# Optimization experiments

Measured on AMD Instinct MI355X. Metric: run time of the kernel, lower is better.

The kernel has to match this reference:

```python
import jax, jax.numpy as jnp
import numpy as np

N_NODES = 100000
N_EDGES = 1600000
IN_CH, HID, EMB = 128, 64, 32


def _glorot(key, shape):
    lim = np.sqrt(6.0 / (shape[0] + shape[1])).astype(np.float32)
    return jax.random.uniform(key, shape, jnp.float32, -lim, lim)


def setup_inputs() -> dict:
    key = jax.random.key(0)
    ks = jax.random.split(key, 5)
    x = jax.random.normal(ks[0], (N_NODES, IN_CH), dtype=jnp.float32)
    edges = jax.random.randint(ks[1], (2, N_EDGES), 0, N_NODES)
    W1 = _glorot(ks[2], (IN_CH, HID)); b1 = jnp.zeros((HID,), jnp.float32)
    W2 = _glorot(ks[3], (HID, EMB)); b2 = jnp.zeros((EMB,), jnp.float32)
    W3 = _glorot(ks[4], (HID, EMB)); b3 = jnp.zeros((EMB,), jnp.float32)
    return {"x": x, "edges": edges, "W1": W1, "b1": b1,
            "W2": W2, "b2": b2, "W3": W3, "b3": b3}


def reference(x, edges, W1, b1, W2, b2, W3, b3):
    N = x.shape[0]
    # GCNConv default: add self-loops, symmetric D^-1/2 A D^-1/2 normalization
    loop = jnp.arange(N, dtype=edges.dtype)
    src = jnp.concatenate([edges[0], loop])  # [E+N] message sources
    dst = jnp.concatenate([edges[1], loop])  # [E+N] message targets
    deg = jax.ops.segment_sum(jnp.ones_like(dst, dtype=x.dtype), dst, num_segments=N)
    dinv = jnp.where(deg > 0, jax.lax.rsqrt(deg), 0.0)
    norm = dinv[src] * dinv[dst]  # [E+N], cached across the three convs (cached=True)

    def gcn(h, W, b):
        h = h @ W                                  # [N, out]
        msg = h[src] * norm[:, None]               # gather + edge scale
        return jax.ops.segment_sum(msg, dst, num_segments=N) + b  # scatter-add

    h = jax.nn.relu(gcn(x, W1, b1))
    return gcn(h, W2, b2), gcn(h, W3, b3)
```

## Files before the change

### kernel.cpp

```cpp
#include <hip/hip_runtime.h>

#define NN 100000
#define NE 1600000
#define NB 391
#define CHUNK 4096
#define NCHUNK 391

typedef __attribute__((ext_vector_type(8))) short short8_t;
typedef __attribute__((ext_vector_type(4))) float float4_t;

__device__ inline unsigned short f2bf(float f) {
    unsigned int u = __float_as_uint(f);
    unsigned int r = u + 0x7fffu + ((u >> 16) & 1u);
    return (unsigned short)(r >> 16);
}
__device__ inline float bf_lo(unsigned int u) { return __uint_as_float(u << 16); }
__device__ inline float bf_hi(unsigned int u) { return __uint_as_float(u & 0xffff0000u); }

__global__ __launch_bounds__(256) void k_hist(const int* __restrict__ dst,
                                              int* __restrict__ bhist) {
    __shared__ int lh[NB];
    int t = threadIdx.x;
    for (int i = t; i < NB; i += 256) lh[i] = 0;
    __syncthreads();
    for (int e = blockIdx.x * 256 + t; e < NE; e += 256 * 256)
        atomicAdd(&lh[dst[e] >> 8], 1);
    __syncthreads();
    for (int i = t; i < NB; i += 256)
        if (lh[i]) atomicAdd(&bhist[i], lh[i]);
}

__global__ __launch_bounds__(256) void k_scanb(const int* __restrict__ bhist,
                                               int* __restrict__ boff,
                                               int* __restrict__ bcur) {
    __shared__ int sh[256];
    int t = threadIdx.x;
    int base = t * 2;
    int v0 = (base + 0 < NB) ? bhist[base + 0] : 0;
    int v1 = (base + 1 < NB) ? bhist[base + 1] : 0;
    int tsum = v0 + v1;
    sh[t] = tsum;
    __syncthreads();
    for (int d = 1; d < 256; d <<= 1) {
        int x = (t >= d) ? sh[t - d] : 0;
        __syncthreads();
        sh[t] += x;
        __syncthreads();
    }
    int excl = sh[t] - tsum;
    if (base + 0 < NB) { boff[base + 0] = excl;      bcur[base + 0] = excl; }
    if (base + 1 < NB) { boff[base + 1] = excl + v0; bcur[base + 1] = excl + v0; }
    if (t == 255) boff[NB] = sh[255];
}

__global__ __launch_bounds__(512) void k_bscatter(const int* __restrict__ src,
                                                  const int* __restrict__ dst,
                                                  int* __restrict__ bcur,
                                                  unsigned int* __restrict__ pairs) {
    __shared__ int lh[NB];
    __shared__ int lbase[NB];
    int t = threadIdx.x;
    int e0 = blockIdx.x * CHUNK;
    int e1 = min(e0 + CHUNK, NE);
    for (int i = t; i < NB; i += 512) lh[i] = 0;
    __syncthreads();
    for (int e = e0 + t; e < e1; e += 512)
        atomicAdd(&lh[dst[e] >> 8], 1);
    __syncthreads();
    int rot = (int)((blockIdx.x * 97u) % NB);
    for (int i = t; i < NB; i += 512) {
        int ii = i + rot; if (ii >= NB) ii -= NB;
        int h = lh[ii];
        lbase[ii] = h ? atomicAdd(&bcur[ii], h) : 0;
    }
    __syncthreads();
    for (int i = t; i < NB; i += 512) lh[i] = 0;
    __syncthreads();
    for (int e = e0 + t; e < e1; e += 512) {
        int d = dst[e];
        int b = d >> 8;
        int r = atomicAdd(&lh[b], 1);
        pairs[lbase[b] + r] = (unsigned int)src[e] | ((unsigned int)(d & 255) << 17);
    }
}

__global__ __launch_bounds__(256) void k_fine(const unsigned int* __restrict__ pairs,
                                              const int* __restrict__ boff,
                                              int* __restrict__ csr_off,
                                              int* __restrict__ csr_src,
                                              float* __restrict__ dinv) {
    __shared__ int lcnt[256];
    __shared__ int sc[256];
    __shared__ int lofs[256];
    int t = threadIdx.x;
    int b = blockIdx.x;
    int n0 = b << 8;
    int nnode = min(256, NN - n0);
    int bO = boff[b], bE = boff[b + 1];

    lcnt[t] = 0;
    __syncthreads();
    for (int e = bO + t; e < bE; e += 256)
        atomicAdd(&lcnt[pairs[e] >> 17], 1);
    __syncthreads();
    sc[t] = lcnt[t];
    __syncthreads();
    for (int d = 1; d < 256; d <<= 1) {
        int x = (t >= d) ? sc[t - d] : 0;
        __syncthreads();
        sc[t] += x;
        __syncthreads();
    }
    {
        int excl = sc[t] - lcnt[t];
        lofs[t] = excl;
        if (t < nnode) {
            int n = n0 + t;
            csr_off[n] = bO + excl;
            dinv[n] = rsqrtf(1.0f + (float)lcnt[t]);
        }
        lcnt[t] = 0;
    }
    if (b == NB - 1 && t == 0) csr_off[NN] = NE;
    __syncthreads();
    for (int e = bO + t; e < bE; e += 256) {
        unsigned int w = pairs[e];
        int li = (int)(w >> 17);
        int r = atomicAdd(&lcnt[li], 1);
        csr_src[bO + lofs[li] + r] = (int)(w & 0x1FFFFu);
    }
}

__global__ __launch_bounds__(256) void k_w1t(const float* __restrict__ W1,
                                             unsigned short* __restrict__ wtb) {
    int f = blockIdx.x * 256 + threadIdx.x;
    int c = f >> 7, k = f & 127;
    wtb[f] = f2bf(W1[k * 64 + c]);
}

__global__ __launch_bounds__(512) void k_gemm1(const float* __restrict__ x,
                                               const unsigned short* __restrict__ wtb,
                                               const float* __restrict__ dinv,
                                               unsigned short* __restrict__ t1b) {
    __shared__ __align__(16) unsigned short lx[128 * 136];
    __shared__ __align__(16) unsigned short lw[64 * 136];
    __shared__ float sdinv[128];
    const int t = threadIdx.x;
    const int row0 = blockIdx.x * 128;
    const int nrows = min(128, NN - row0);

    #pragma unroll
    for (int i = 0; i < 8; ++i) {
        int f = t + i * 512;
        int r = f >> 5, c4 = f & 31;
        float4 v = make_float4(0.f, 0.f, 0.f, 0.f);
        if (r < nrows) v = ((const float4*)(x + (size_t)(row0 + r) * 128))[c4];
        ushort4 o;
        o.x = f2bf(v.x); o.y = f2bf(v.y); o.z = f2bf(v.z); o.w = f2bf(v.w);
        *(ushort4*)&lx[r * 136 + c4 * 4] = o;
    }
    #pragma unroll
    for (int i = 0; i < 2; ++i) {
        int f = t + i * 512;
        int c = f >> 4, c8 = f & 15;
        uint4 v = ((const uint4*)wtb)[f];
        *(uint4*)&lw[c * 136 + c8 * 8] = v;
    }
    if (t < 128) sdinv[t] = (row0 + t < NN) ? dinv[row0 + t] : 0.f;
    __syncthreads();

    const int w = t >> 6, l = t & 63;
    const int m15 = l & 15, kg = l >> 4;
    const unsigned short* pa = &lx[(w * 16 + m15) * 136 + kg * 8];
    const unsigned short* pb = &lw[m15 * 136 + kg * 8];

    float4_t acc[4];
    #pragma unroll
    for (int cb = 0; cb < 4; ++cb) acc[cb] = (float4_t){0.f, 0.f, 0.f, 0.f};

    #pragma unroll
    for (int ks = 0; ks < 4; ++ks) {
        short8_t a = *(const short8_t*)(pa + ks * 32);
        #pragma unroll
        for (int cb = 0; cb < 4; ++cb) {
            short8_t b = *(const short8_t*)(pb + cb * (16 * 136) + ks * 32);
            acc[cb] = __builtin_amdgcn_mfma_f32_16x16x32_bf16(a, b, acc[cb], 0, 0, 0);
        }
    }

    #pragma unroll
    for (int r = 0; r < 4; ++r) {
        int lrow = w * 16 + kg * 4 + r;
        if (lrow < nrows) {
            float dn = sdinv[lrow];
            size_t grow = (size_t)(row0 + lrow);
            #pragma unroll
            for (int cb = 0; cb < 4; ++cb)
                t1b[grow * 64 + cb * 16 + m15] = f2bf(acc[cb][r] * dn);
        }
    }
}

template <bool RELU>
__global__ __launch_bounds__(256) void k_gather8(const int* __restrict__ off,
                                                 const int* __restrict__ csr,
                                                 const float* __restrict__ dinv,
                                                 const unsigned short* __restrict__ hb,
                                                 const float* __restrict__ bias,
                                                 unsigned int* __restrict__ outp) {
    int idx = blockIdx.x * 256 + threadIdx.x;
    int n = idx >> 3;
    if (n >= NN) return;
    int c8 = idx & 7;
    const uint4* h4 = (const uint4*)hb;
    float dn = dinv[n];
    float acc[8];
    {
        uint4 v = h4[(size_t)n * 8 + c8];
        acc[0] = bf_lo(v.x); acc[1] = bf_hi(v.x);
        acc[2] = bf_lo(v.y); acc[3] = bf_hi(v.y);
        acc[4] = bf_lo(v.z); acc[5] = bf_hi(v.z);
        acc[6] = bf_lo(v.w); acc[7] = bf_hi(v.w);
    }
    int b = off[n], e = off[n + 1];
    int i = b;
    if (i < e) {
        int s = csr[i];
        for (++i; i < e; ++i) {
            int sn = csr[i];
            uint4 v = h4[(size_t)s * 8 + c8];
            acc[0] += bf_lo(v.x); acc[1] += bf_hi(v.x);
            acc[2] += bf_lo(v.y); acc[3] += bf_hi(v.y);
            acc[4] += bf_lo(v.z); acc[5] += bf_hi(v.z);
            acc[6] += bf_lo(v.w); acc[7] += bf_hi(v.w);
            s = sn;
        }
        uint4 v = h4[(size_t)s * 8 + c8];
        acc[0] += bf_lo(v.x); acc[1] += bf_hi(v.x);
        acc[2] += bf_lo(v.y); acc[3] += bf_hi(v.y);
        acc[4] += bf_lo(v.z); acc[5] += bf_hi(v.z);
        acc[6] += bf_lo(v.w); acc[7] += bf_hi(v.w);
    }
    float o[8];
    if (RELU) {
        float4 b0 = ((const float4*)bias)[c8 * 2];
        float4 b1 = ((const float4*)bias)[c8 * 2 + 1];
        o[0] = dn * fmaxf(dn * acc[0] + b0.x, 0.f);
        o[1] = dn * fmaxf(dn * acc[1] + b0.y, 0.f);
        o[2] = dn * fmaxf(dn * acc[2] + b0.z, 0.f);
        o[3] = dn * fmaxf(dn * acc[3] + b0.w, 0.f);
        o[4] = dn * fmaxf(dn * acc[4] + b1.x, 0.f);
        o[5] = dn * fmaxf(dn * acc[5] + b1.y, 0.f);
        o[6] = dn * fmaxf(dn * acc[6] + b1.z, 0.f);
        o[7] = dn * fmaxf(dn * acc[7] + b1.w, 0.f);
    } else {
        #pragma unroll
        for (int j = 0; j < 8; ++j) o[j] = dn * acc[j];
    }
    uint4 p;
    p.x = (unsigned int)f2bf(o[0]) | ((unsigned int)f2bf(o[1]) << 16);
    p.y = (unsigned int)f2bf(o[2]) | ((unsigned int)f2bf(o[3]) << 16);
    p.z = (unsigned int)f2bf(o[4]) | ((unsigned int)f2bf(o[5]) << 16);
    p.w = (unsigned int)f2bf(o[6]) | ((unsigned int)f2bf(o[7]) << 16);
    ((uint4*)outp)[(size_t)n * 8 + c8] = p;
}

__global__ __launch_bounds__(256) void k_gg2(const int* __restrict__ off,
                                             const int* __restrict__ csr,
                                             const float* __restrict__ dinv,
                                             const unsigned short* __restrict__ hb,
                                             const float* __restrict__ W2, const float* __restrict__ b2,
                                             const float* __restrict__ W3, const float* __restrict__ b3,
                                             float* __restrict__ out) {
    __shared__ float as_[64][72];
    __shared__ float wc[64 * 64];
    __shared__ float bc[64];
    const int t = threadIdx.x;
    const int row0 = blockIdx.x * 64;
    const int nrows = min(64, NN - row0);

    #pragma unroll
    for (int i = 0; i < 16; ++i) {
        int f = t + i * 256;
        int k = f >> 6, c = f & 63;
        wc[f] = (c < 32) ? W2[k * 32 + c] : W3[k * 32 + (c - 32)];
    }
    if (t < 64) bc[t] = (t < 32) ? b2[t] : b3[t - 32];

    {
        const int nl = t >> 2;
        const int n = row0 + nl;
        const int c16 = t & 3;
        float acc[16];
        if (n < NN) {
            const uint4* h4 = (const uint4*)hb;
            float dn = dinv[n];
            size_t base = (size_t)n * 8 + c16 * 2;
            uint4 v0 = h4[base], v1 = h4[base + 1];
            acc[0]  = bf_lo(v0.x); acc[1]  = bf_hi(v0.x);
            acc[2]  = bf_lo(v0.y); acc[3]  = bf_hi(v0.y);
            acc[4]  = bf_lo(v0.z); acc[5]  = bf_hi(v0.z);
            acc[6]  = bf_lo(v0.w); acc[7]  = bf_hi(v0.w);
            acc[8]  = bf_lo(v1.x); acc[9]  = bf_hi(v1.x);
            acc[10] = bf_lo(v1.y); acc[11] = bf_hi(v1.y);
            acc[12] = bf_lo(v1.z); acc[13] = bf_hi(v1.z);
            acc[14] = bf_lo(v1.w); acc[15] = bf_hi(v1.w);
            int b = off[n], e = off[n + 1];
            int i = b;
            if (i < e) {
                int s = csr[i];
                for (++i; i < e; ++i) {
                    int sn = csr[i];
                    size_t sb = (size_t)s * 8 + c16 * 2;
                    uint4 w0 = h4[sb], w1 = h4[sb + 1];
                    acc[0]  += bf_lo(w0.x); acc[1]  += bf_hi(w0.x);
                    acc[2]  += bf_lo(w0.y); acc[3]  += bf_hi(w0.y);
                    acc[4]  += bf_lo(w0.z); acc[5]  += bf_hi(w0.z);
                    acc[6]  += bf_lo(w0.w); acc[7]  += bf_hi(w0.w);
                    acc[8]  += bf_lo(w1.x); acc[9]  += bf_hi(w1.x);
                    acc[10] += bf_lo(w1.y); acc[11] += bf_hi(w1.y);
                    acc[12] += bf_lo(w1.z); acc[13] += bf_hi(w1.z);
                    acc[14] += bf_lo(w1.w); acc[15] += bf_hi(w1.w);
                    s = sn;
                }
                size_t sb = (size_t)s * 8 + c16 * 2;
                uint4 w0 = h4[sb], w1 = h4[sb + 1];
                acc[0]  += bf_lo(w0.x); acc[1]  += bf_hi(w0.x);
                acc[2]  += bf_lo(w0.y); acc[3]  += bf_hi(w0.y);
                acc[4]  += bf_lo(w0.z); acc[5]  += bf_hi(w0.z);
                acc[6]  += bf_lo(w0.w); acc[7]  += bf_hi(w0.w);
                acc[8]  += bf_lo(w1.x); acc[9]  += bf_hi(w1.x);
                acc[10] += bf_lo(w1.y); acc[11] += bf_hi(w1.y);
                acc[12] += bf_lo(w1.z); acc[13] += bf_hi(w1.z);
                acc[14] += bf_lo(w1.w); acc[15] += bf_hi(w1.w);
            }
            #pragma unroll
            for (int j = 0; j < 16; ++j) acc[j] *= dn;
        } else {
            #pragma unroll
            for (int j = 0; j < 16; ++j) acc[j] = 0.f;
        }
        float* dp = &as_[nl][c16 * 16];
        #pragma unroll
        for (int j = 0; j < 16; ++j) dp[j] = acc[j];
    }
    __syncthreads();

    const int tc = t & 15;
    const int tr = t >> 4;
    float acc[4][4];
    #pragma unroll
    for (int i = 0; i < 4; ++i)
        #pragma unroll
        for (int j = 0; j < 4; ++j) acc[i][j] = 0.f;

    #pragma unroll 4
    for (int k = 0; k < 64; ++k) {
        float4 wv = *(const float4*)&wc[k * 64 + tc * 4];
        #pragma unroll
        for (int i = 0; i < 4; ++i) {
            float xv = as_[tr * 4 + i][k];
            acc[i][0] += xv * wv.x; acc[i][1] += xv * wv.y;
            acc[i][2] += xv * wv.z; acc[i][3] += xv * wv.w;
        }
    }
    const int c0 = tc * 4;
    float4 bias = *(float4*)&bc[c0];
    #pragma unroll
    for (int i = 0; i < 4; ++i) {
        int r = tr * 4 + i;
        if (r < nrows) {
            float4 o = make_float4(acc[i][0] + bias.x, acc[i][1] + bias.y,
                                   acc[i][2] + bias.z, acc[i][3] + bias.w);
            size_t row = (size_t)(row0 + r);
            float* p = (tc < 8) ? (out + row * 32 + c0)
                                : (out + (size_t)NN * 32 + row * 32 + (c0 - 32));
            *(float4*)p = o;
        }
    }
}

extern "C" void kernel_launch(void* const* d_in, const int* in_sizes, int n_in,
                              void* d_out, int out_size, void* d_ws, size_t ws_size,
                              hipStream_t stream) {
    const float* x  = (const float*)d_in[0];
    const int* edges = (const int*)d_in[1];
    const float* W1 = (const float*)d_in[2];
    const float* b1 = (const float*)d_in[3];
    const float* W2 = (const float*)d_in[4];
    const float* b2 = (const float*)d_in[5];
    const float* W3 = (const float*)d_in[6];
    const float* b3 = (const float*)d_in[7];
    float* out = (float*)d_out;

    const int* srcs = edges;
    const int* dsts = edges + NE;

    int*   csr_off = (int*)d_ws;
    float* dinv    = (float*)((int*)d_ws + 100004);
    int*   csr_src = (int*)d_ws + 200004;
    int*   bhist   = (int*)d_ws + 1800004;
    int*   boff    = (int*)d_ws + 1800396;
    int*   bcur    = (int*)d_ws + 1800788;
    unsigned short* wtb = (unsigned short*)((int*)d_ws + 1801184);
    unsigned int*   pairs = (unsigned int*)((int*)d_ws + 1805280);
    unsigned short* t1b   = (unsigned short*)pairs;
    unsigned short* h1b   = (unsigned short*)((int*)d_ws + 5005280);

    dim3 blk(256);
    const int gN8 = (NN * 8 + 255) / 256;
    const int gT  = (NN + 63) / 64;
    const int gT1 = (NN + 127) / 128;

    hipMemsetAsync(bhist, 0, NB * sizeof(int), stream);
    k_hist<<<256, blk, 0, stream>>>(dsts, bhist);
    k_w1t<<<32, blk, 0, stream>>>(W1, wtb);
    k_scanb<<<1, blk, 0, stream>>>(bhist, boff, bcur);
    k_bscatter<<<NCHUNK, dim3(512), 0, stream>>>(srcs, dsts, bcur, pairs);
    k_fine<<<NB, blk, 0, stream>>>(pairs, boff, csr_off, csr_src, dinv);

    k_gemm1<<<gT1, dim3(512), 0, stream>>>(x, wtb, dinv, t1b);
    k_gather8<true><<<gN8, blk, 0, stream>>>(csr_off, csr_src, dinv, t1b, b1,
                                             (unsigned int*)h1b);
    k_gg2<<<gT, blk, 0, stream>>>(csr_off, csr_src, dinv, h1b, W2, b2, W3, b3, out);
}
```

Before: 158.4 us.

## Fuse GEMM1 with edge bucket scatter and apply source dinv in gather

Merges the first dense GEMM and the edge bucket scatter into one heterogeneous launch: every third block does scatter work and the other two compute GEMM tiles, so GEMM1 no longer waits for the CSR build. Because the GEMM no longer depends on dinv, the source-side normalization moves into the layer-1 gather as a per-edge dinv[src] load and multiply. The gather and gg2 loops are also unrolled by two with dual accumulators to raise memory-level parallelism. The cost is an extra random dinv load per edge in layer 1, plus workspace buffers reordered so t1b and pairs no longer alias.

```diff
diff --git a/kernel.cpp b/kernel.cpp
--- a/kernel.cpp
+++ b/kernel.cpp
@@ -53,34 +53,104 @@
     if (t == 255) boff[NB] = sh[255];
 }
 
-__global__ __launch_bounds__(512) void k_bscatter(const int* __restrict__ src,
-                                                  const int* __restrict__ dst,
-                                                  int* __restrict__ bcur,
-                                                  unsigned int* __restrict__ pairs) {
-    __shared__ int lh[NB];
-    __shared__ int lbase[NB];
-    int t = threadIdx.x;
-    int e0 = blockIdx.x * CHUNK;
-    int e1 = min(e0 + CHUNK, NE);
-    for (int i = t; i < NB; i += 512) lh[i] = 0;
-    __syncthreads();
-    for (int e = e0 + t; e < e1; e += 512)
-        atomicAdd(&lh[dst[e] >> 8], 1);
-    __syncthreads();
-    int rot = (int)((blockIdx.x * 97u) % NB);
-    for (int i = t; i < NB; i += 512) {
-        int ii = i + rot; if (ii >= NB) ii -= NB;
-        int h = lh[ii];
-        lbase[ii] = h ? atomicAdd(&bcur[ii], h) : 0;
-    }
-    __syncthreads();
-    for (int i = t; i < NB; i += 512) lh[i] = 0;
-    __syncthreads();
-    for (int e = e0 + t; e < e1; e += 512) {
-        int d = dst[e];
-        int b = d >> 8;
-        int r = atomicAdd(&lh[b], 1);
-        pairs[lbase[b] + r] = (unsigned int)src[e] | ((unsigned int)(d & 255) << 17);
+__global__ __launch_bounds__(256) void k_w1t(const float* __restrict__ W1,
+                                             unsigned short* __restrict__ wtb) {
+    int f = blockIdx.x * 256 + threadIdx.x;
+    int c = f >> 7, k = f & 127;
+    wtb[f] = f2bf(W1[k * 64 + c]);
+}
+
+__global__ __launch_bounds__(512) void k_fuse(const float* __restrict__ x,
+                                              const unsigned short* __restrict__ wtb,
+                                              unsigned short* __restrict__ t1b,
+                                              const int* __restrict__ src,
+                                              const int* __restrict__ dst,
+                                              int* __restrict__ bcur,
+                                              unsigned int* __restrict__ pairs) {
+    __shared__ __align__(16) unsigned char smem[52224];
+    const int b = blockIdx.x;
+    const int t = threadIdx.x;
+
+    if ((b % 3) == 2) {
+        int* lh    = (int*)smem;
+        int* lbase = lh + NB;
+        int e0 = (b / 3) * CHUNK;
+        int e1 = min(e0 + CHUNK, NE);
+        for (int i = t; i < NB; i += 512) lh[i] = 0;
+        __syncthreads();
+        for (int e = e0 + t; e < e1; e += 512)
+            atomicAdd(&lh[dst[e] >> 8], 1);
+        __syncthreads();
+        int rot = (int)(((unsigned)(b / 3) * 97u) % NB);
+        for (int i = t; i < NB; i += 512) {
+            int ii = i + rot; if (ii >= NB) ii -= NB;
+            int h = lh[ii];
+            lbase[ii] = h ? atomicAdd(&bcur[ii], h) : 0;
+        }
+        __syncthreads();
+        for (int i = t; i < NB; i += 512) lh[i] = 0;
+        __syncthreads();
+        for (int e = e0 + t; e < e1; e += 512) {
+            int d = dst[e];
+            int bk = d >> 8;
+            int r = atomicAdd(&lh[bk], 1);
+            pairs[lbase[bk] + r] = (unsigned int)src[e] | ((unsigned int)(d & 255) << 17);
+        }
+    } else {
+        unsigned short* lx = (unsigned short*)smem;
+        unsigned short* lw = (unsigned short*)(smem + 34816);
+        const int tile = 2 * (b / 3) + (b % 3);
+        const int row0 = tile * 128;
+        const int nrows = min(128, NN - row0);
+
+        #pragma unroll
+        for (int i = 0; i < 8; ++i) {
+            int f = t + i * 512;
+            int r = f >> 5, c4 = f & 31;
+            float4 v = make_float4(0.f, 0.f, 0.f, 0.f);
+            if (r < nrows) v = ((const float4*)(x + (size_t)(row0 + r) * 128))[c4];
+            ushort4 o;
+            o.x = f2bf(v.x); o.y = f2bf(v.y); o.z = f2bf(v.z); o.w = f2bf(v.w);
+            *(ushort4*)&lx[r * 136 + c4 * 4] = o;
+        }
+        #pragma unroll
+        for (int i = 0; i < 2; ++i) {
+            int f = t + i * 512;
+            int c = f >> 4, c8 = f & 15;
+            uint4 v = ((const uint4*)wtb)[f];
+            *(uint4*)&lw[c * 136 + c8 * 8] = v;
+        }
+        __syncthreads();
+
+        const int w = t >> 6, l = t & 63;
+        const int m15 = l & 15, kg = l >> 4;
+        const unsigned short* pa = &lx[(w * 16 + m15) * 136 + kg * 8];
+        const unsigned short* pb = &lw[m15 * 136 + kg * 8];
+
+        float4_t acc[4];
+        #pragma unroll
+        for (int cb = 0; cb < 4; ++cb) acc[cb] = (float4_t){0.f, 0.f, 0.f, 0.f};
+
+        #pragma unroll
+        for (int ks = 0; ks < 4; ++ks) {
+            short8_t a = *(const short8_t*)(pa + ks * 32);
+            #pragma unroll
+            for (int cb = 0; cb < 4; ++cb) {
+                short8_t bb = *(const short8_t*)(pb + cb * (16 * 136) + ks * 32);
+                acc[cb] = __builtin_amdgcn_mfma_f32_16x16x32_bf16(a, bb, acc[cb], 0, 0, 0);
+            }
+        }
+
+        #pragma unroll
+        for (int r = 0; r < 4; ++r) {
+            int lrow = w * 16 + kg * 4 + r;
+            if (lrow < nrows) {
+                size_t grow = (size_t)(row0 + lrow);
+                #pragma unroll
+                for (int cb = 0; cb < 4; ++cb)
+                    t1b[grow * 64 + cb * 16 + m15] = f2bf(acc[cb][r]);
+            }
+        }
     }
 }
 
@@ -131,77 +201,6 @@
     }
 }
 
-__global__ __launch_bounds__(256) void k_w1t(const float* __restrict__ W1,
-                                             unsigned short* __restrict__ wtb) {
-    int f = blockIdx.x * 256 + threadIdx.x;
-    int c = f >> 7, k = f & 127;
-    wtb[f] = f2bf(W1[k * 64 + c]);
-}
-
-__global__ __launch_bounds__(512) void k_gemm1(const float* __restrict__ x,
-                                               const unsigned short* __restrict__ wtb,
-                                               const float* __restrict__ dinv,
-                                               unsigned short* __restrict__ t1b) {
-    __shared__ __align__(16) unsigned short lx[128 * 136];
-    __shared__ __align__(16) unsigned short lw[64 * 136];
-    __shared__ float sdinv[128];
-    const int t = threadIdx.x;
-    const int row0 = blockIdx.x * 128;
-    const int nrows = min(128, NN - row0);
-
-    #pragma unroll
-    for (int i = 0; i < 8; ++i) {
-        int f = t + i * 512;
-        int r = f >> 5, c4 = f & 31;
-        float4 v = make_float4(0.f, 0.f, 0.f, 0.f);
-        if (r < nrows) v = ((const float4*)(x + (size_t)(row0 + r) * 128))[c4];
-        ushort4 o;
-        o.x = f2bf(v.x); o.y = f2bf(v.y); o.z = f2bf(v.z); o.w = f2bf(v.w);
-        *(ushort4*)&lx[r * 136 + c4 * 4] = o;
-    }
-    #pragma unroll
-    for (int i = 0; i < 2; ++i) {
-        int f = t + i * 512;
-        int c = f >> 4, c8 = f & 15;
-        uint4 v = ((const uint4*)wtb)[f];
-        *(uint4*)&lw[c * 136 + c8 * 8] = v;
-    }
-    if (t < 128) sdinv[t] = (row0 + t < NN) ? dinv[row0 + t] : 0.f;
-    __syncthreads();
-
-    const int w = t >> 6, l = t & 63;
-    const int m15 = l & 15, kg = l >> 4;
-    const unsigned short* pa = &lx[(w * 16 + m15) * 136 + kg * 8];
-    const unsigned short* pb = &lw[m15 * 136 + kg * 8];
-
-    float4_t acc[4];
-    #pragma unroll
-    for (int cb = 0; cb < 4; ++cb) acc[cb] = (float4_t){0.f, 0.f, 0.f, 0.f};
-
-    #pragma unroll
-    for (int ks = 0; ks < 4; ++ks) {
-        short8_t a = *(const short8_t*)(pa + ks * 32);
-        #pragma unroll
-        for (int cb = 0; cb < 4; ++cb) {
-            short8_t b = *(const short8_t*)(pb + cb * (16 * 136) + ks * 32);
-            acc[cb] = __builtin_amdgcn_mfma_f32_16x16x32_bf16(a, b, acc[cb], 0, 0, 0);
-        }
-    }
-
-    #pragma unroll
-    for (int r = 0; r < 4; ++r) {
-        int lrow = w * 16 + kg * 4 + r;
-        if (lrow < nrows) {
-            float dn = sdinv[lrow];
-            size_t grow = (size_t)(row0 + lrow);
-            #pragma unroll
-            for (int cb = 0; cb < 4; ++cb)
-                t1b[grow * 64 + cb * 16 + m15] = f2bf(acc[cb][r] * dn);
-        }
-    }
-}
-
-template <bool RELU>
 __global__ __launch_bounds__(256) void k_gather8(const int* __restrict__ off,
                                                  const int* __restrict__ csr,
                                                  const float* __restrict__ dinv,
@@ -214,49 +213,52 @@
     int c8 = idx & 7;
     const uint4* h4 = (const uint4*)hb;
     float dn = dinv[n];
-    float acc[8];
+    float a0[8], a1[8];
     {
         uint4 v = h4[(size_t)n * 8 + c8];
-        acc[0] = bf_lo(v.x); acc[1] = bf_hi(v.x);
-        acc[2] = bf_lo(v.y); acc[3] = bf_hi(v.y);
-        acc[4] = bf_lo(v.z); acc[5] = bf_hi(v.z);
-        acc[6] = bf_lo(v.w); acc[7] = bf_hi(v.w);
+        a0[0] = dn * bf_lo(v.x); a0[1] = dn * bf_hi(v.x);
+        a0[2] = dn * bf_lo(v.y); a0[3] = dn * bf_hi(v.y);
+        a0[4] = dn * bf_lo(v.z); a0[5] = dn * bf_hi(v.z);
+        a0[6] = dn * bf_lo(v.w); a0[7] = dn * bf_hi(v.w);
+        #pragma unroll
+        for (int j = 0; j < 8; ++j) a1[j] = 0.f;
     }
     int b = off[n], e = off[n + 1];
     int i = b;
+    for (; i + 1 < e; i += 2) {
+        int s0 = csr[i], s1 = csr[i + 1];
+        float w0 = dinv[s0], w1 = dinv[s1];
+        uint4 v0 = h4[(size_t)s0 * 8 + c8];
+        uint4 v1 = h4[(size_t)s1 * 8 + c8];
+        a0[0] += w0 * bf_lo(v0.x); a0[1] += w0 * bf_hi(v0.x);
+        a0[2] += w0 * bf_lo(v0.y); a0[3] += w0 * bf_hi(v0.y);
+        a0[4] += w0 * bf_lo(v0.z); a0[5] += w0 * bf_hi(v0.z);
+        a0[6] += w0 * bf_lo(v0.w); a0[7] += w0 * bf_hi(v0.w);
+        a1[0] += w1 * bf_lo(v1.x); a1[1] += w1 * bf_hi(v1.x);
+        a1[2] += w1 * bf_lo(v1.y); a1[3] += w1 * bf_hi(v1.y);
+        a1[4] += w1 * bf_lo(v1.z); a1[5] += w1 * bf_hi(v1.z);
+        a1[6] += w1 * bf_lo(v1.w); a1[7] += w1 * bf_hi(v1.w);
+    }
     if (i < e) {
         int s = csr[i];
-        for (++i; i < e; ++i) {
-            int sn = csr[i];
-            uint4 v = h4[(size_t)s * 8 + c8];
-            acc[0] += bf_lo(v.x); acc[1] += bf_hi(v.x);
-            acc[2] += bf_lo(v.y); acc[3] += bf_hi(v.y);
-            acc[4] += bf_lo(v.z); acc[5] += bf_hi(v.z);
-            acc[6] += bf_lo(v.w); acc[7] += bf_hi(v.w);
-            s = sn;
-        }
+        float w = dinv[s];
         uint4 v = h4[(size_t)s * 8 + c8];
-        acc[0] += bf_lo(v.x); acc[1] += bf_hi(v.x);
-        acc[2] += bf_lo(v.y); acc[3] += bf_hi(v.y);
-        acc[4] += bf_lo(v.z); acc[5] += bf_hi(v.z);
-        acc[6] += bf_lo(v.w); acc[7] += bf_hi(v.w);
-    }
+        a0[0] += w * bf_lo(v.x); a0[1] += w * bf_hi(v.x);
+        a0[2] += w * bf_lo(v.y); a0[3] += w * bf_hi(v.y);
+        a0[4] += w * bf_lo(v.z); a0[5] += w * bf_hi(v.z);
+        a0[6] += w * bf_lo(v.w); a0[7] += w * bf_hi(v.w);
+    }
+    float4 b0 = ((const float4*)bias)[c8 * 2];
+    float4 b1v = ((const float4*)bias)[c8 * 2 + 1];
     float o[8];
-    if (RELU) {
-        float4 b0 = ((const float4*)bias)[c8 * 2];
-        float4 b1 = ((const float4*)bias)[c8 * 2 + 1];
-        o[0] = dn * fmaxf(dn * acc[0] + b0.x, 0.f);
-        o[1] = dn * fmaxf(dn * acc[1] + b0.y, 0.f);
-        o[2] = dn * fmaxf(dn * acc[2] + b0.z, 0.f);
-        o[3] = dn * fmaxf(dn * acc[3] + b0.w, 0.f);
-        o[4] = dn * fmaxf(dn * acc[4] + b1.x, 0.f);
-        o[5] = dn * fmaxf(dn * acc[5] + b1.y, 0.f);
-        o[6] = dn * fmaxf(dn * acc[6] + b1.z, 0.f);
-        o[7] = dn * fmaxf(dn * acc[7] + b1.w, 0.f);
-    } else {
-        #pragma unroll
-        for (int j = 0; j < 8; ++j) o[j] = dn * acc[j];
-    }
+    o[0] = dn * fmaxf(dn * (a0[0] + a1[0]) + b0.x, 0.f);
+    o[1] = dn * fmaxf(dn * (a0[1] + a1[1]) + b0.y, 0.f);
+    o[2] = dn * fmaxf(dn * (a0[2] + a1[2]) + b0.z, 0.f);
+    o[3] = dn * fmaxf(dn * (a0[3] + a1[3]) + b0.w, 0.f);
+    o[4] = dn * fmaxf(dn * (a0[4] + a1[4]) + b1v.x, 0.f);
+    o[5] = dn * fmaxf(dn * (a0[5] + a1[5]) + b1v.y, 0.f);
+    o[6] = dn * fmaxf(dn * (a0[6] + a1[6]) + b1v.z, 0.f);
+    o[7] = dn * fmaxf(dn * (a0[7] + a1[7]) + b1v.w, 0.f);
     uint4 p;
     p.x = (unsigned int)f2bf(o[0]) | ((unsigned int)f2bf(o[1]) << 16);
     p.y = (unsigned int)f2bf(o[2]) | ((unsigned int)f2bf(o[3]) << 16);
@@ -307,23 +309,31 @@
             acc[14] = bf_lo(v1.w); acc[15] = bf_hi(v1.w);
             int b = off[n], e = off[n + 1];
             int i = b;
+            for (; i + 1 < e; i += 2) {
+                int s0 = csr[i], s1 = csr[i + 1];
+                size_t sb0 = (size_t)s0 * 8 + c16 * 2;
+                size_t sb1 = (size_t)s1 * 8 + c16 * 2;
+                uint4 w0 = h4[sb0], w1 = h4[sb0 + 1];
+                uint4 u0 = h4[sb1], u1 = h4[sb1 + 1];
+                acc[0]  += bf_lo(w0.x); acc[1]  += bf_hi(w0.x);
+                acc[2]  += bf_lo(w0.y); acc[3]  += bf_hi(w0.y);
+                acc[4]  += bf_lo(w0.z); acc[5]  += bf_hi(w0.z);
+                acc[6]  += bf_lo(w0.w); acc[7]  += bf_hi(w0.w);
+                acc[8]  += bf_lo(w1.x); acc[9]  += bf_hi(w1.x);
+                acc[10] += bf_lo(w1.y); acc[11] += bf_hi(w1.y);
+                acc[12] += bf_lo(w1.z); acc[13] += bf_hi(w1.z);
+                acc[14] += bf_lo(w1.w); acc[15] += bf_hi(w1.w);
+                acc[0]  += bf_lo(u0.x); acc[1]  += bf_hi(u0.x);
+                acc[2]  += bf_lo(u0.y); acc[3]  += bf_hi(u0.y);
+                acc[4]  += bf_lo(u0.z); acc[5]  += bf_hi(u0.z);
+                acc[6]  += bf_lo(u0.w); acc[7]  += bf_hi(u0.w);
+                acc[8]  += bf_lo(u1.x); acc[9]  += bf_hi(u1.x);
+                acc[10] += bf_lo(u1.y); acc[11] += bf_hi(u1.y);
+                acc[12] += bf_lo(u1.z); acc[13] += bf_hi(u1.z);
+                acc[14] += bf_lo(u1.w); acc[15] += bf_hi(u1.w);
+            }
             if (i < e) {
-                int s = csr[i];
-                for (++i; i < e; ++i) {
-                    int sn = csr[i];
-                    size_t sb = (size_t)s * 8 + c16 * 2;
-                    uint4 w0 = h4[sb], w1 = h4[sb + 1];
-                    acc[0]  += bf_lo(w0.x); acc[1]  += bf_hi(w0.x);
-                    acc[2]  += bf_lo(w0.y); acc[3]  += bf_hi(w0.y);
-                    acc[4]  += bf_lo(w0.z); acc[5]  += bf_hi(w0.z);
-                    acc[6]  += bf_lo(w0.w); acc[7]  += bf_hi(w0.w);
-                    acc[8]  += bf_lo(w1.x); acc[9]  += bf_hi(w1.x);
-                    acc[10] += bf_lo(w1.y); acc[11] += bf_hi(w1.y);
-                    acc[12] += bf_lo(w1.z); acc[13] += bf_hi(w1.z);
-                    acc[14] += bf_lo(w1.w); acc[15] += bf_hi(w1.w);
-                    s = sn;
-                }
-                size_t sb = (size_t)s * 8 + c16 * 2;
+                size_t sb = (size_t)csr[i] * 8 + c16 * 2;
                 uint4 w0 = h4[sb], w1 = h4[sb + 1];
                 acc[0]  += bf_lo(w0.x); acc[1]  += bf_hi(w0.x);
                 acc[2]  += bf_lo(w0.y); acc[3]  += bf_hi(w0.y);
@@ -403,24 +413,24 @@
     int*   boff    = (int*)d_ws + 1800396;
     int*   bcur    = (int*)d_ws + 1800788;
     unsigned short* wtb = (unsigned short*)((int*)d_ws + 1801184);
-    unsigned int*   pairs = (unsigned int*)((int*)d_ws + 1805280);
-    unsigned short* t1b   = (unsigned short*)pairs;
-    unsigned short* h1b   = (unsigned short*)((int*)d_ws + 5005280);
+    unsigned short* t1b = (unsigned short*)((int*)d_ws + 1805280);
+    unsigned int*   pairs = (unsigned int*)((int*)d_ws + 5005280);
+    unsigned short* h1b   = (unsigned short*)pairs;
 
     dim3 blk(256);
     const int gN8 = (NN * 8 + 255) / 256;
     const int gT  = (NN + 63) / 64;
-    const int gT1 = (NN + 127) / 128;
 
     hipMemsetAsync(bhist, 0, NB * sizeof(int), stream);
     k_hist<<<256, blk, 0, stream>>>(dsts, bhist);
     k_w1t<<<32, blk, 0, stream>>>(W1, wtb);
     k_scanb<<<1, blk, 0, stream>>>(bhist, boff, bcur);
-    k_bscatter<<<NCHUNK, dim3(512), 0, stream>>>(srcs, dsts, bcur, pairs);
+
+    k_fuse<<<3 * NCHUNK, dim3(512), 0, stream>>>(x, wtb, t1b, srcs, dsts, bcur, pairs);
+
     k_fine<<<NB, blk, 0, stream>>>(pairs, boff, csr_off, csr_src, dinv);
 
-    k_gemm1<<<gT1, dim3(512), 0, stream>>>(x, wtb, dinv, t1b);
-    k_gather8<true><<<gN8, blk, 0, stream>>>(csr_off, csr_src, dinv, t1b, b1,
-                                             (unsigned int*)h1b);
+    k_gather8<<<gN8, blk, 0, stream>>>(csr_off, csr_src, dinv, t1b, b1,
+                                       (unsigned int*)h1b);
     k_gg2<<<gT, blk, 0, stream>>>(csr_off, csr_src, dinv, h1b, W2, b2, W3, b3, out);
 }
```

Measured after the change: 152.1 us. 1.04x faster.
